# Kernel tuning notes

Measured on AMD Instinct MI355X. Metric: run time of the kernel, lower is better.

## Reference

```python
import jax, jax.numpy as jnp
import numpy as np

G = 3  # group_num
EPS = 1e-5


def _ln(x, g, b):
    m = x.mean(-1, keepdims=True)
    v = x.var(-1, keepdims=True)
    return (x - m) / jnp.sqrt(v + EPS) * g + b


def _gcm(x, w_qk, b_qk, ct_w1, ct_b1, ct_g, ct_be, ct_w2, ct_b2,
         lw_w1, lw_b1, lw_g, lw_be, lw_w2, lw_b2):
    # x: [B, 768, H, W] (pre-concatenated group feature)
    b, c, h, w = x.shape
    gc = c // G
    # channel shuffle: b (g c) h w -> b (c g) h w
    xs = x.reshape(b, G, gc, h, w).transpose(0, 2, 1, 3, 4).reshape(b, c, h, w)
    out = xs.reshape(b, G, gc, h, w)            # b g c h w
    value = out.reshape(b, G, gc, h * w)        # b g c n
    # fc_qk (Linear gc->1) over the channel axis, softmax over spatial n
    logits = jnp.einsum('bgcn,c->bgn', value, w_qk) + b_qk
    attn = jax.nn.softmax(logits, axis=-1)       # b g n
    context = jnp.einsum('bgcn,bgn->bgc', value, attn)  # b g c
    lvl_context = context.reshape(b, c)          # b (g c)
    # ctx_transform: Linear -> LN -> ReLU -> Linear
    h1 = jax.nn.relu(_ln(context @ ct_w1.T + ct_b1, ct_g, ct_be))
    ctx = h1 @ ct_w2.T + ct_b2                   # b g c
    # lvl_weight: Linear -> LN -> ReLU -> Linear -> Sigmoid
    l1 = jax.nn.relu(_ln(lvl_context @ lw_w1.T + lw_b1, lw_g, lw_be))
    lvlw = jax.nn.sigmoid(l1 @ lw_w2.T + lw_b2)  # b g (=3)
    ctx = ctx * lvlw[:, :, None]
    return (out + ctx[:, :, :, None, None]).sum(axis=1)  # b c_g h w


def setup_inputs() -> dict:
    key = jax.random.key(0)
    ks = jax.random.split(key, 16)
    B = 8
    sizes = [(128, 128), (64, 64), (32, 32), (16, 16)]
    inp = {}
    for i, (h, w) in enumerate(sizes):
        inp[f'g{i}'] = jax.random.normal(ks[i], (B, 768, h, w), jnp.float32)
    inp['x_last'] = jax.random.normal(ks[4], (B, 256, 8, 8), jnp.float32)
    s = 0.05
    inp['w_qk'] = jax.random.normal(ks[5], (4, 256), jnp.float32) * s
    inp['b_qk'] = jax.random.normal(ks[6], (4,), jnp.float32) * s
    inp['ct_w1'] = jax.random.normal(ks[7], (4, 64, 256), jnp.float32) * s
    inp['ct_b1'] = jax.random.normal(ks[8], (4, 64), jnp.float32) * s
    inp['ct_g'] = jnp.ones((4, 64), jnp.float32)
    inp['ct_be'] = jnp.zeros((4, 64), jnp.float32)
    inp['ct_w2'] = jax.random.normal(ks[9], (4, 256, 64), jnp.float32) * s
    inp['ct_b2'] = jax.random.normal(ks[10], (4, 256), jnp.float32) * s
    inp['lw_w1'] = jax.random.normal(ks[11], (4, 768, 768), jnp.float32) * s
    inp['lw_b1'] = jax.random.normal(ks[12], (4, 768), jnp.float32) * s
    inp['lw_g'] = jnp.ones((4, 768), jnp.float32)
    inp['lw_be'] = jnp.zeros((4, 768), jnp.float32)
    inp['lw_w2'] = jax.random.normal(ks[13], (4, 3, 768), jnp.float32) * s
    inp['lw_b2'] = jax.random.normal(ks[14], (4, 3), jnp.float32) * s
    return inp


def reference(g0, g1, g2, g3, x_last, w_qk, b_qk, ct_w1, ct_b1, ct_g, ct_be,
              ct_w2, ct_b2, lw_w1, lw_b1, lw_g, lw_be, lw_w2, lw_b2):
    outs = []
    for i, g in enumerate([g0, g1, g2, g3]):
        outs.append(_gcm(g, w_qk[i], b_qk[i], ct_w1[i], ct_b1[i], ct_g[i],
                         ct_be[i], ct_w2[i], ct_b2[i], lw_w1[i], lw_b1[i],
                         lw_g[i], lw_be[i], lw_w2[i], lw_b2[i]))
    return (*outs, x_last)
```

## Files before the change

### kernel.cpp

```cpp
#include <hip/hip_runtime.h>

#define NB 8
#define NWG 680
#define PSTRIDE 772

typedef float f4 __attribute__((ext_vector_type(4)));

__device__ __forceinline__ f4 ntload(const float* p) {
  return __builtin_nontemporal_load((const f4*)p);
}
__device__ __forceinline__ void ntstore(float* p, f4 v) {
  __builtin_nontemporal_store(v, (f4*)p);
}
__device__ __forceinline__ float hsum(f4 v) { return v.x + v.y + v.z + v.w; }

struct KFArgs {
  const float* x[4];
  float* outp[4];
  float* partial;
  int N[4];
};

__global__ __launch_bounds__(512, 4) void kf_fused(KFArgs a, const float* __restrict__ wqk_all) {
  __shared__ float red[768];
  __shared__ float se[96];
  __shared__ float zred[96];

  int wg = blockIdx.x;
  int lvl, b, idx;
  if (wg < 512)      { lvl = 0; b = wg >> 6;            idx = wg & 63; }
  else if (wg < 640) { int r = wg - 512; lvl = 1; b = r >> 4; idx = r & 15; }
  else if (wg < 672) { int r = wg - 640; lvl = 2; b = r >> 2; idx = r & 3; }
  else               { int r = wg - 672; lvl = 3; b = r;      idx = 0; }
  int N = a.N[lvl];
  int col0 = idx * 256;
  const float* __restrict__ xb = a.x[lvl] + (size_t)b * 768 * N;
  float* __restrict__ outb = a.outp[lvl] + (size_t)b * 256 * N;
  int tid = threadIdx.x;
  int snq = tid & 7, oq = tid >> 3, wv = tid >> 6;

  int srow[4][3];
  float wq[4];
#pragma unroll
  for (int j = 0; j < 4; ++j) {
    int c2 = oq + 64 * j;
    wq[j] = wqk_all[lvl * 256 + c2];
#pragma unroll
    for (int k = 0; k < 3; ++k) {
      int f = c2 + (k << 8);
      srow[j][k] = (f % 3) * 256 + f / 3;
    }
  }

  float acc[4][3] = {{0.f, 0.f, 0.f}, {0.f, 0.f, 0.f}, {0.f, 0.f, 0.f}, {0.f, 0.f, 0.f}};
  float zacc = 0.f;

  for (int tt = 0; tt < 8; ++tt) {
    int n0 = col0 + tt * 32 + snq * 4;
    f4 reg[4][3];
#pragma unroll
    for (int j = 0; j < 4; ++j)
#pragma unroll
      for (int k = 0; k < 3; ++k)
        reg[j][k] = ntload(xb + (size_t)srow[j][k] * N + n0);

    f4 pg[3] = {{0.f, 0.f, 0.f, 0.f}, {0.f, 0.f, 0.f, 0.f}, {0.f, 0.f, 0.f, 0.f}};
#pragma unroll
    for (int j = 0; j < 4; ++j)
#pragma unroll
      for (int k = 0; k < 3; ++k)
        pg[k] += reg[j][k] * wq[j];
#pragma unroll
    for (int k = 0; k < 3; ++k) {
#pragma unroll
      for (int m = 8; m <= 32; m <<= 1) {
        pg[k].x += __shfl_xor(pg[k].x, m);
        pg[k].y += __shfl_xor(pg[k].y, m);
        pg[k].z += __shfl_xor(pg[k].z, m);
        pg[k].w += __shfl_xor(pg[k].w, m);
      }
    }
    if ((tid & 63) < 8) {
#pragma unroll
      for (int k = 0; k < 3; ++k)
        *(f4*)(red + (wv * 24 + k * 8 + snq) * 4) = pg[k];
    }
    __syncthreads();
    if (tid < 96) {
      int k = tid >> 5, col = tid & 31;
      float l = 0.f;
#pragma unroll
      for (int w = 0; w < 8; ++w) l += red[(w * 24 + k * 8) * 4 + col];
      float e = __expf(l);
      se[k * 32 + col] = e;
      zacc += e;
    }
    __syncthreads();
#pragma unroll
    for (int j = 0; j < 4; ++j) {
      f4 ov = reg[j][0] + reg[j][1] + reg[j][2];
      *(f4*)(outb + (size_t)(oq + 64 * j) * N + n0) = ov;
#pragma unroll
      for (int k = 0; k < 3; ++k) {
        f4 p = reg[j][k] * *(const f4*)(se + k * 32 + snq * 4);
        acc[j][k] += hsum(p);
      }
    }
  }

  float* pw = a.partial + (size_t)wg * PSTRIDE;
#pragma unroll
  for (int j = 0; j < 4; ++j)
#pragma unroll
    for (int k = 0; k < 3; ++k) {
      float v = acc[j][k];
      v += __shfl_xor(v, 1);
      v += __shfl_xor(v, 2);
      v += __shfl_xor(v, 4);
      if (snq == 0) pw[k * 256 + oq + 64 * j] = v;
    }
  if (tid < 96) zred[tid] = zacc;
  __syncthreads();
  if (tid < 3) {
    float z = 0.f;
#pragma unroll
    for (int i = 0; i < 32; ++i) z += zred[tid * 32 + i];
    pw[768 + tid] = z;
  }
}

__device__ __forceinline__ float blk_sum256(float v, float* sr4) {
  for (int o = 32; o; o >>= 1) v += __shfl_xor(v, o);
  __syncthreads();
  if ((threadIdx.x & 63) == 0) sr4[threadIdx.x >> 6] = v;
  __syncthreads();
  return sr4[0] + sr4[1] + sr4[2] + sr4[3];
}

__global__ __launch_bounds__(256) void k4_mlp(
    const float* __restrict__ partial,
    const float* __restrict__ ct_w1, const float* __restrict__ ct_b1,
    const float* __restrict__ ct_g,  const float* __restrict__ ct_be,
    const float* __restrict__ ct_w2, const float* __restrict__ ct_b2,
    const float* __restrict__ lw_w1, const float* __restrict__ lw_b1,
    const float* __restrict__ lw_g,  const float* __restrict__ lw_be,
    const float* __restrict__ lw_w2, const float* __restrict__ lw_b2,
    float* __restrict__ add_all) {
  int b = blockIdx.x, lvl = blockIdx.y;
  int t = threadIdx.x;
  static const int cnt_[4] = {64, 16, 4, 1};
  static const int base_[4] = {0, 512, 640, 672};
  int cnt = cnt_[lvl];
  int wg0 = base_[lvl] + b * cnt;

  const float* w1 = ct_w1 + lvl * 64 * 256;
  const float* b1 = ct_b1 + lvl * 64;
  const float* cg = ct_g + lvl * 64;
  const float* cbe = ct_be + lvl * 64;
  const float* w2 = ct_w2 + lvl * 256 * 64;
  const float* b2 = ct_b2 + lvl * 256;
  const float* W1 = lw_w1 + (size_t)lvl * 768 * 768;
  const float* B1 = lw_b1 + lvl * 768;
  const float* Lg = lw_g + lvl * 768;
  const float* Lbe = lw_be + lvl * 768;
  const float* W2 = lw_w2 + lvl * 3 * 768;
  const float* B2 = lw_b2 + lvl * 3;
  float* addp = add_all + ((size_t)lvl * NB + b) * 256;

  __shared__ float sctx[768];
  __shared__ float sh1[3][64];
  __shared__ float sl1[768];
  __shared__ float slvlw[3];
  __shared__ float sr4[4];
  __shared__ float sZ[3];

  float s0 = 0.f, s1 = 0.f, s2 = 0.f;
  for (int w = 0; w < cnt; ++w) {
    const float* pw = partial + (size_t)(wg0 + w) * PSTRIDE;
    s0 += pw[t];
    s1 += pw[t + 256];
    s2 += pw[t + 512];
  }
  if (t < 3) {
    float z = 0.f;
    for (int w = 0; w < cnt; ++w) z += partial[(size_t)(wg0 + w) * PSTRIDE + 768 + t];
    sZ[t] = z;
  }
  __syncthreads();
  sctx[t] = s0 / sZ[0];
  sctx[t + 256] = s1 / sZ[1];
  sctx[t + 512] = s2 / sZ[2];
  __syncthreads();

  if (t < 192) {
    int g = t >> 6, j = t & 63;
    const f4* w4 = (const f4*)(w1 + j * 256);
    const f4* c4 = (const f4*)(sctx + g * 256);
    f4 acc = {0.f, 0.f, 0.f, 0.f};
#pragma unroll 8
    for (int k = 0; k < 64; ++k) acc += c4[k] * w4[k];
    sh1[g][j] = hsum(acc) + b1[j];
  }
  __syncthreads();
  int wv = t >> 6, ln = t & 63;
  if (wv < 3) {
    float v = sh1[wv][ln];
    float s = v;
    for (int o = 32; o; o >>= 1) s += __shfl_xor(s, o);
    float mean = s * (1.f / 64.f);
    float d = v - mean;
    float q = d * d;
    for (int o = 32; o; o >>= 1) q += __shfl_xor(q, o);
    float var = q * (1.f / 64.f);
    float y = d * rsqrtf(var + 1e-5f) * cg[ln] + cbe[ln];
    sh1[wv][ln] = fmaxf(y, 0.f);
  }
  __syncthreads();
  float l1v[3];
#pragma unroll
  for (int r = 0; r < 3; ++r) {
    int j = t + r * 256;
    const f4* W4 = (const f4*)(W1 + (size_t)j * 768);
    const f4* s4 = (const f4*)sctx;
    f4 acc = {0.f, 0.f, 0.f, 0.f};
#pragma unroll 8
    for (int k = 0; k < 192; ++k) acc += s4[k] * W4[k];
    l1v[r] = hsum(acc) + B1[j];
  }
  float S = blk_sum256(l1v[0] + l1v[1] + l1v[2], sr4);
  float mean = S * (1.f / 768.f);
  float q = 0.f;
#pragma unroll
  for (int r = 0; r < 3; ++r) { float d = l1v[r] - mean; q += d * d; }
  float var = blk_sum256(q, sr4) * (1.f / 768.f);
  float inv = rsqrtf(var + 1e-5f);
#pragma unroll
  for (int r = 0; r < 3; ++r) {
    int j = t + r * 256;
    float y = (l1v[r] - mean) * inv * Lg[j] + Lbe[j];
    sl1[j] = fmaxf(y, 0.f);
  }
  __syncthreads();
  if (wv < 3) {
    float acc = 0.f;
    for (int j = ln; j < 768; j += 64) acc = fmaf(sl1[j], W2[wv * 768 + j], acc);
    for (int o = 32; o; o >>= 1) acc += __shfl_xor(acc, o);
    if (ln == 0) slvlw[wv] = 1.f / (1.f + __expf(-(acc + B2[wv])));
  }
  __syncthreads();
  {
    int c2 = t;
    float a = 0.f;
#pragma unroll
    for (int g = 0; g < 3; ++g) {
      const f4* w4 = (const f4*)(w2 + c2 * 64);
      const f4* h4 = (const f4*)(sh1[g]);
      f4 acc = {0.f, 0.f, 0.f, 0.f};
#pragma unroll
      for (int j = 0; j < 16; ++j) acc += h4[j] * w4[j];
      a += (hsum(acc) + b2[c2]) * slvlw[g];
    }
    addp[c2] = a;
  }
}

__global__ __launch_bounds__(256) void k5_add(float* __restrict__ out,
                                              const float* __restrict__ add_all,
                                              const float* __restrict__ xlast) {
  size_t f4i = (size_t)blockIdx.x * 256 + threadIdx.x;
  if (f4i >= 11141120) {
    size_t r = f4i - 11141120;
    f4 v = ntload(xlast + (r << 2));
    ntstore(out + (f4i << 2), v);
    return;
  }
  int lvl, lgN2;
  size_t base;
  if (f4i < 8388608)       { lvl = 0; base = 0;        lgN2 = 12; }
  else if (f4i < 10485760) { lvl = 1; base = 8388608;  lgN2 = 10; }
  else if (f4i < 11010048) { lvl = 2; base = 10485760; lgN2 = 8;  }
  else                     { lvl = 3; base = 11010048; lgN2 = 6;  }
  size_t lf4 = f4i - base;
  int bc = (int)(lf4 >> lgN2);
  float a = add_all[lvl * 2048 + bc];
  float* p = out + (f4i << 2);
  f4 v = *(const f4*)p;
  v += a;
  ntstore(p, v);
}

extern "C" void kernel_launch(void* const* d_in, const int* in_sizes, int n_in,
                              void* d_out, int out_size, void* d_ws, size_t ws_size,
                              hipStream_t stream) {
  const float* gx[4] = {(const float*)d_in[0], (const float*)d_in[1],
                        (const float*)d_in[2], (const float*)d_in[3]};
  const float* x_last = (const float*)d_in[4];
  const float* w_qk = (const float*)d_in[5];
  const float* ct_w1 = (const float*)d_in[7];
  const float* ct_b1 = (const float*)d_in[8];
  const float* ct_g  = (const float*)d_in[9];
  const float* ct_be = (const float*)d_in[10];
  const float* ct_w2 = (const float*)d_in[11];
  const float* ct_b2 = (const float*)d_in[12];
  const float* lw_w1 = (const float*)d_in[13];
  const float* lw_b1 = (const float*)d_in[14];
  const float* lw_g  = (const float*)d_in[15];
  const float* lw_be = (const float*)d_in[16];
  const float* lw_w2 = (const float*)d_in[17];
  const float* lw_b2 = (const float*)d_in[18];
  float* out = (float*)d_out;
  float* ws = (float*)d_ws;

  static const int Ns[4] = {16384, 4096, 1024, 256};
  static const size_t outOff[4] = {0, 33554432, 41943040, 44040192};

  float* partb = ws;
  float* addb  = ws + NWG * PSTRIDE;

  KFArgs af;
  for (int i = 0; i < 4; ++i) {
    af.x[i] = gx[i];
    af.outp[i] = out + outOff[i];
    af.N[i] = Ns[i];
  }
  af.partial = partb;

  kf_fused<<<dim3(NWG), dim3(512), 0, stream>>>(af, w_qk);
  k4_mlp<<<dim3(NB, 4), dim3(256), 0, stream>>>(partb, ct_w1, ct_b1, ct_g, ct_be,
                                                ct_w2, ct_b2, lw_w1, lw_b1, lw_g,
                                                lw_be, lw_w2, lw_b2, addb);
  k5_add<<<dim3(43648), dim3(256), 0, stream>>>(out, addb, x_last);
}
```

Measured before the change: 329.8 us.

## Double-buffer tile loads and replace second barrier with redundant per-thread softmax

Software-pipelines the fused pass so the next 32-column tile's global loads are issued into a second register buffer while the current tile is reduced and written. The shared reduction buffer is double-buffered, and every thread now recomputes the summed logits and exponentials for its own columns, which removes the second block barrier and the shared exp buffer. Launch bounds drop the occupancy hint from 4 to 2 blocks per CU to make room for the extra registers. The cost is higher register pressure, lower occupancy and redundant exp and LDS reads in every thread.

```diff
diff --git a/kernel.cpp b/kernel.cpp
--- a/kernel.cpp
+++ b/kernel.cpp
@@ -21,10 +21,9 @@
   int N[4];
 };
 
-__global__ __launch_bounds__(512, 4) void kf_fused(KFArgs a, const float* __restrict__ wqk_all) {
-  __shared__ float red[768];
-  __shared__ float se[96];
-  __shared__ float zred[96];
+__global__ __launch_bounds__(512, 2) void kf_fused(KFArgs a, const float* __restrict__ wqk_all) {
+  __shared__ float red[2][768];
+  __shared__ float zl[24];
 
   int wg = blockIdx.x;
   int lvl, b, idx;
@@ -53,23 +52,28 @@
   }
 
   float acc[4][3] = {{0.f, 0.f, 0.f}, {0.f, 0.f, 0.f}, {0.f, 0.f, 0.f}, {0.f, 0.f, 0.f}};
-  float zacc = 0.f;
-
-  for (int tt = 0; tt < 8; ++tt) {
+  float za[3] = {0.f, 0.f, 0.f};
+
+  f4 A[12], B[12];
+
+  auto issue = [&](f4* buf, int tile) {
+    int n0 = col0 + tile * 32 + snq * 4;
+#pragma unroll
+    for (int j = 0; j < 4; ++j)
+#pragma unroll
+      for (int k = 0; k < 3; ++k)
+        buf[j * 3 + k] = ntload(xb + (size_t)srow[j][k] * N + n0);
+  };
+
+  auto body = [&](f4* cur, f4* nxt, int tt, bool pre) {
     int n0 = col0 + tt * 32 + snq * 4;
-    f4 reg[4][3];
+    if (pre) issue(nxt, tt + 1);
+    f4 pg[3] = {{0.f, 0.f, 0.f, 0.f}, {0.f, 0.f, 0.f, 0.f}, {0.f, 0.f, 0.f, 0.f}};
 #pragma unroll
     for (int j = 0; j < 4; ++j)
 #pragma unroll
       for (int k = 0; k < 3; ++k)
-        reg[j][k] = ntload(xb + (size_t)srow[j][k] * N + n0);
-
-    f4 pg[3] = {{0.f, 0.f, 0.f, 0.f}, {0.f, 0.f, 0.f, 0.f}, {0.f, 0.f, 0.f, 0.f}};
-#pragma unroll
-    for (int j = 0; j < 4; ++j)
-#pragma unroll
-      for (int k = 0; k < 3; ++k)
-        pg[k] += reg[j][k] * wq[j];
+        pg[k] += cur[j * 3 + k] * wq[j];
 #pragma unroll
     for (int k = 0; k < 3; ++k) {
 #pragma unroll
@@ -80,32 +84,44 @@
         pg[k].w += __shfl_xor(pg[k].w, m);
       }
     }
+    float* rb = red[tt & 1];
     if ((tid & 63) < 8) {
 #pragma unroll
       for (int k = 0; k < 3; ++k)
-        *(f4*)(red + (wv * 24 + k * 8 + snq) * 4) = pg[k];
-    }
-    __syncthreads();
-    if (tid < 96) {
-      int k = tid >> 5, col = tid & 31;
-      float l = 0.f;
-#pragma unroll
-      for (int w = 0; w < 8; ++w) l += red[(w * 24 + k * 8) * 4 + col];
-      float e = __expf(l);
-      se[k * 32 + col] = e;
-      zacc += e;
-    }
-    __syncthreads();
+        *(f4*)(rb + (wv * 24 + k * 8 + snq) * 4) = pg[k];
+    }
+    asm volatile("s_waitcnt lgkmcnt(0)" ::: "memory");
+    __builtin_amdgcn_sched_barrier(0);
+    __builtin_amdgcn_s_barrier();
+    __builtin_amdgcn_sched_barrier(0);
+    f4 sev[3];
+#pragma unroll
+    for (int k = 0; k < 3; ++k) {
+      f4 s = {0.f, 0.f, 0.f, 0.f};
+#pragma unroll
+      for (int w = 0; w < 8; ++w) s += *(const f4*)(rb + (w * 24 + k * 8 + snq) * 4);
+      f4 e;
+      e.x = __expf(s.x); e.y = __expf(s.y); e.z = __expf(s.z); e.w = __expf(s.w);
+      sev[k] = e;
+    }
+    if (tid < 8) {
+#pragma unroll
+      for (int k = 0; k < 3; ++k) za[k] += hsum(sev[k]);
+    }
 #pragma unroll
     for (int j = 0; j < 4; ++j) {
-      f4 ov = reg[j][0] + reg[j][1] + reg[j][2];
+      f4 ov = cur[j * 3 + 0] + cur[j * 3 + 1] + cur[j * 3 + 2];
       *(f4*)(outb + (size_t)(oq + 64 * j) * N + n0) = ov;
 #pragma unroll
-      for (int k = 0; k < 3; ++k) {
-        f4 p = reg[j][k] * *(const f4*)(se + k * 32 + snq * 4);
-        acc[j][k] += hsum(p);
-      }
-    }
+      for (int k = 0; k < 3; ++k)
+        acc[j][k] += hsum(cur[j * 3 + k] * sev[k]);
+    }
+  };
+
+  issue(A, 0);
+  for (int tt = 0; tt < 8; tt += 2) {
+    body(A, B, tt, true);
+    body(B, A, tt + 1, tt + 1 < 7);
   }
 
   float* pw = a.partial + (size_t)wg * PSTRIDE;
@@ -119,12 +135,15 @@
       v += __shfl_xor(v, 4);
       if (snq == 0) pw[k * 256 + oq + 64 * j] = v;
     }
-  if (tid < 96) zred[tid] = zacc;
+  if (tid < 8) {
+#pragma unroll
+    for (int k = 0; k < 3; ++k) zl[tid * 3 + k] = za[k];
+  }
   __syncthreads();
   if (tid < 3) {
     float z = 0.f;
 #pragma unroll
-    for (int i = 0; i < 32; ++i) z += zred[tid * 32 + i];
+    for (int s = 0; s < 8; ++s) z += zl[s * 3 + tid];
     pw[768 + tid] = z;
   }
 }
```

Result: faster. 304.8 us (-7.6%).
